# Kernel optimization log

Hardware: AMD Instinct MI355X
Metric: run time of the kernel (lower is better)

## Reference

```python
import jax, jax.numpy as jnp
import numpy as np

B, C, L, H, W = 4, 128, 8, 64, 64

def setup_inputs() -> dict:
    key = jax.random.key(0)
    ks = jax.random.split(key, 9)
    s = 0.05
    return {
        'feats': jax.random.normal(ks[0], (B, C, L, H, W), jnp.float32),
        'proj_w': jax.random.normal(ks[1], (C, C, L), jnp.float32) * s,  # Conv3d kernel (band,1,1) collapsing l
        'proj_b': jax.random.normal(ks[2], (C,), jnp.float32) * s,
        'w1': jax.random.normal(ks[3], (C, C), jnp.float32) * s,
        'b1': jax.random.normal(ks[4], (C,), jnp.float32) * s,
        'w2': jax.random.normal(ks[5], (C, C), jnp.float32) * s,
        'b2': jax.random.normal(ks[6], (C,), jnp.float32) * s,
        'w3': jax.random.normal(ks[7], (C, C), jnp.float32) * s,
        'b3': jax.random.normal(ks[8], (C,), jnp.float32) * s,
        'alpha': jnp.zeros((1,), jnp.float32),
    }

def reference(feats, proj_w, proj_b, w1, b1, w2, b2, w3, b3, alpha):
    b, c, l, h, w = feats.shape
    hw = h * w
    # CVT3D_2D_SA: 3D->2D projection, conv3d kernel (l,1,1) then squeeze
    f2d = jnp.einsum('bclhw,ocl->bohw', feats, proj_w) + proj_b[None, :, None, None]
    # 1x1 conv projections -> (b, c, hw)
    x = f2d.reshape(b, c, hw)
    q = jnp.einsum('bcn,oc->bon', x, w1) + b1[None, :, None]
    k = jnp.einsum('bcn,oc->bon', x, w2) + b2[None, :, None]
    v = jnp.einsum('bcn,oc->bon', x, w3) + b3[None, :, None]
    # scores[b,n,m] = sum_c q[b,c,n] * k[b,c,m]; softmax over m (dim=-1)
    scores = jnp.einsum('bcn,bcm->bnm', q, k)
    attn = jax.nn.softmax(scores, axis=-1)
    # feat_e[b,c,n] = sum_m v[b,c,m] * attn[b,n,m]
    feat_e = jnp.einsum('bcm,bnm->bcn', v, attn).reshape(b, c, h, w)
    # original computes out = alpha*feat_e + f2d but returns feat_e
    return feat_e
```

## Files before the change

kernel.cpp:

```cpp
#include <hip/hip_runtime.h>
#include <stdint.h>

typedef _Float16 h8 __attribute__((ext_vector_type(8)));
typedef _Float16 h4 __attribute__((ext_vector_type(4)));
typedef float f32x4 __attribute__((ext_vector_type(4)));
typedef float f32x16 __attribute__((ext_vector_type(16)));
typedef uint32_t u32x4 __attribute__((ext_vector_type(4)));

#if __has_builtin(__builtin_amdgcn_exp2f)
#define EXP2(x) __builtin_amdgcn_exp2f(x)
#else
#define EXP2(x) exp2f(x)
#endif

#if __has_builtin(__builtin_amdgcn_permlane32_swap)
#define HAVE_PLSWAP 1
#else
#define HAVE_PLSWAP 0
#endif

#define WS_PWH  0u
#define WS_WH   262144u
#define WS_BC   600064u
#define WS_F2D  1048576u
#define WS_OP   5242880u
#define WS_QKVT 38797312u
#define WS_VT   47185920u
#define WS_MLM  0u
#define WS_MLL  524288u

__device__ __forceinline__ void gll16(const void* g, void* l) {
  __builtin_amdgcn_global_load_lds((const __attribute__((address_space(1))) unsigned int*)g,
                                   (__attribute__((address_space(3))) unsigned int*)l, 16, 0, 0);
}

__global__ void k_cvt(const float* __restrict__ pw, const float* __restrict__ pb,
                      const float* __restrict__ w1, const float* __restrict__ b1,
                      const float* __restrict__ w2, const float* __restrict__ b2,
                      const float* __restrict__ w3, const float* __restrict__ b3,
                      _Float16* __restrict__ PWh, _Float16* __restrict__ Wh,
                      float* __restrict__ bc)
{
  const float LOG2E = 1.4426950408889634f;
  int idx = blockIdx.x * 256 + threadIdx.x;
  if (idx < 131072) {
    PWh[idx] = (_Float16)pw[idx];
  } else {
    int j = idx - 131072;
    if (j < 49152) {
      int g = j >> 14, rem = j & 16383;
      const float* wg = (g == 0) ? w1 : (g == 1 ? w2 : w3);
      float v = wg[rem];
      if (g == 0) v *= LOG2E;
      Wh[j] = (_Float16)v;
    }
  }
  if (idx < 384) {
    int g = idx >> 7, o = idx & 127;
    const float* wg = (g == 0) ? w1 : (g == 1 ? w2 : w3);
    const float* bg = (g == 0) ? b1 : (g == 1 ? b2 : b3);
    float s = bg[o];
    for (int c = 0; c < 128; ++c) s += wg[o * 128 + c] * pb[c];
    if (g == 0) s *= LOG2E;
    bc[idx] = s;
  }
}

#define FG1_LDS 51200
__global__ __launch_bounds__(256) void k_fg1(const float* __restrict__ feats,
                                             const _Float16* __restrict__ PWh,
                                             _Float16* __restrict__ f2d)
{
  extern __shared__ char smem[];
  const int t = threadIdx.x, lane = t & 63, w = t >> 6;
  const int lo = lane & 15, hi = lane >> 4;
  const int n0 = blockIdx.x * 32, b = blockIdx.y;
  const int wr = w >> 1, wc = w & 1;
  const char* pwc = (const char*)PWh;

  float4 areg[2];
  auto loadA = [&](int s) {
    #pragma unroll
    for (int p = 0; p < 2; ++p) {
      int i = t + p * 256, row = i >> 3, slot = i & 7;
      areg[p] = *(const float4*)(feats + ((size_t)(b * 1024 + s * 64 + row)) * 4096 + n0 + slot * 4);
    }
  };
  auto writeA = [&](int buf) {
    char* base = smem + buf * 9216;
    #pragma unroll
    for (int p = 0; p < 2; ++p) {
      int i = t + p * 256, row = i >> 3, slot = i & 7;
      *(float4*)(base + row * 144 + slot * 16) = areg[p];
    }
  };
  auto gllB = [&](int s, int buf) {
    char* base = smem + 18432 + buf * 16384;
    #pragma unroll
    for (int q = 0; q < 4; ++q) {
      int o = (w * 4 + q) * 8 + (lane >> 3);
      int slot = lane & 7;
      gll16(pwc + (size_t)o * 2048 + s * 128 + ((slot * 16) ^ ((o & 7) << 4)),
            base + (w * 4 + q) * 1024);
    }
  };

  const f32x4 zero4 = {0.f, 0.f, 0.f, 0.f};
  f32x4 acc[4];
  #pragma unroll
  for (int j2 = 0; j2 < 4; ++j2) acc[j2] = zero4;

  loadA(0); writeA(0); gllB(0, 0);
  for (int s = 0; s < 16; ++s) {
    __syncthreads();
    if (s < 15) { loadA(s + 1); gllB(s + 1, (s + 1) & 1); }
    const char* fb = smem + (s & 1) * 9216;
    const char* pb_ = smem + 18432 + (s & 1) * 16384;
    #pragma unroll
    for (int kk = 0; kk < 2; ++kk) {
      const int nl = wr * 16 + lo;
      float f0 = *(const float*)(fb + (kk * 32 + hi * 8 + 0) * 144 + nl * 4);
      float f1 = *(const float*)(fb + (kk * 32 + hi * 8 + 1) * 144 + nl * 4);
      float f2 = *(const float*)(fb + (kk * 32 + hi * 8 + 2) * 144 + nl * 4);
      float f3 = *(const float*)(fb + (kk * 32 + hi * 8 + 3) * 144 + nl * 4);
      float f4 = *(const float*)(fb + (kk * 32 + hi * 8 + 4) * 144 + nl * 4);
      float f5 = *(const float*)(fb + (kk * 32 + hi * 8 + 5) * 144 + nl * 4);
      float f6 = *(const float*)(fb + (kk * 32 + hi * 8 + 6) * 144 + nl * 4);
      float f7 = *(const float*)(fb + (kk * 32 + hi * 8 + 7) * 144 + nl * 4);
      u32x4 ua = { __builtin_bit_cast(uint32_t, __builtin_amdgcn_cvt_pkrtz(f0, f1)),
                   __builtin_bit_cast(uint32_t, __builtin_amdgcn_cvt_pkrtz(f2, f3)),
                   __builtin_bit_cast(uint32_t, __builtin_amdgcn_cvt_pkrtz(f4, f5)),
                   __builtin_bit_cast(uint32_t, __builtin_amdgcn_cvt_pkrtz(f6, f7)) };
      h8 af = __builtin_bit_cast(h8, ua);
      h8 bf[4];
      #pragma unroll
      for (int j2 = 0; j2 < 4; ++j2) {
        int o = wc * 64 + j2 * 16 + lo;
        bf[j2] = *(const h8*)(pb_ + o * 128 + ((kk * 64 + hi * 16) ^ ((o & 7) << 4)));
      }
      #pragma unroll
      for (int j2 = 0; j2 < 4; ++j2)
        acc[j2] = __builtin_amdgcn_mfma_f32_16x16x32_f16(af, bf[j2], acc[j2], 0, 0, 0);
    }
    if (s < 15) writeA((s + 1) & 1);
  }

  #pragma unroll
  for (int j2 = 0; j2 < 4; ++j2) {
    int o = wc * 64 + j2 * 16 + lo;
    #pragma unroll
    for (int r = 0; r < 4; ++r) {
      int n = n0 + wr * 16 + hi * 4 + r;
      f2d[((size_t)(b * 4096 + n)) * 128 + o] = (_Float16)acc[j2][r];
    }
  }
}

__global__ void k_gemm2(const _Float16* __restrict__ f2d, const _Float16* __restrict__ Wh,
                        const float* __restrict__ bc, _Float16* __restrict__ qkvt,
                        _Float16* __restrict__ vt)
{
  extern __shared__ char smem[];
  const int t = threadIdx.x, lane = t & 63, w = t >> 6;
  const int lo = lane & 15, hi = lane >> 4;
  const int bx = blockIdx.x, n0 = blockIdx.y * 128, b = blockIdx.z;
  const int wr = w >> 1, wc = w & 1;
  const int nb = wr * 64, ob = wc * 64;
  const char* f2c = (const char*)f2d;

  #pragma unroll
  for (int q = 0; q < 8; ++q) {
    int c = w * 8 + q;
    int row = c * 4 + (lane >> 4);
    int col = ((lane & 15) * 16) ^ ((row & 7) << 4);
    gll16(f2c + ((size_t)(b * 4096 + n0 + row)) * 256 + col, smem + c * 1024);
    gll16((const char*)Wh + (size_t)(bx * 128 + row) * 256 + col, smem + 32768 + c * 1024);
  }
  __syncthreads();

  const f32x4 zero4 = {0.f, 0.f, 0.f, 0.f};
  f32x4 acc[4][4];
  #pragma unroll
  for (int i2 = 0; i2 < 4; ++i2)
    #pragma unroll
    for (int j2 = 0; j2 < 4; ++j2) acc[i2][j2] = zero4;

  #pragma unroll
  for (int kk = 0; kk < 4; ++kk) {
    const int cb = kk * 64 + hi * 16;
    h8 af[4], bf[4];
    #pragma unroll
    for (int i2 = 0; i2 < 4; ++i2) {
      int row = nb + i2 * 16 + lo;
      af[i2] = *(const h8*)(smem + row * 256 + (cb ^ ((row & 7) << 4)));
    }
    #pragma unroll
    for (int j2 = 0; j2 < 4; ++j2) {
      int row = ob + j2 * 16 + lo;
      bf[j2] = *(const h8*)(smem + 32768 + row * 256 + (cb ^ ((row & 7) << 4)));
    }
    #pragma unroll
    for (int i2 = 0; i2 < 4; ++i2)
      #pragma unroll
      for (int j2 = 0; j2 < 4; ++j2)
        acc[i2][j2] = __builtin_amdgcn_mfma_f32_16x16x32_f16(af[i2], bf[j2], acc[i2][j2], 0, 0, 0);
  }

  if (bx < 2) {
    #pragma unroll
    for (int j2 = 0; j2 < 4; ++j2) {
      int o = bx * 128 + ob + j2 * 16 + lo;
      float bias = bc[o];
      #pragma unroll
      for (int i2 = 0; i2 < 4; ++i2)
        #pragma unroll
        for (int r = 0; r < 4; ++r) {
          int n = n0 + nb + i2 * 16 + hi * 4 + r;
          qkvt[((size_t)(b * 4096 + n)) * 256 + o] = (_Float16)(acc[i2][j2][r] + bias);
        }
    }
  } else {
    __syncthreads();
    #pragma unroll
    for (int j2 = 0; j2 < 4; ++j2) {
      int o = ob + j2 * 16 + lo;
      float bias = bc[256 + o];
      #pragma unroll
      for (int i2 = 0; i2 < 4; ++i2) {
        int nl = nb + i2 * 16 + hi * 4;
        h4 v4;
        #pragma unroll
        for (int r = 0; r < 4; ++r) v4[r] = (_Float16)(acc[i2][j2][r] + bias);
        *(h4*)(smem + o * 272 + nl * 2) = v4;
      }
    }
    __syncthreads();
    #pragma unroll
    for (int p2 = 0; p2 < 8; ++p2) {
      int i = t + p2 * 256, d = i >> 4, ch = i & 15;
      uint4 v = *(const uint4*)(smem + d * 272 + ch * 16);
      *(uint4*)((char*)vt + ((size_t)(b * 128 + d)) * 8192 + (n0 + ch * 8) * 2) = v;
    }
  }
}

#define ATT_LDS 32768
__global__ __launch_bounds__(256, 2) void k_attn_part(const _Float16* __restrict__ qkvt,
                                                      const _Float16* __restrict__ vt,
                                                      _Float16* __restrict__ opart,
                                                      float* __restrict__ mlm,
                                                      float* __restrict__ mll)
{
  extern __shared__ char smem[];
  const int t = threadIdx.x, lane = t & 63, w = t >> 6;
  const int q31 = lane & 31, h2 = lane >> 5;
  const int id = blockIdx.x;
  const int vid = (id & 7) * 128 + (id >> 3);
  const int qt = vid & 31, bp = vid >> 5;
  const int b = bp >> 3, p = bp & 7;
  const int n0 = qt * 128;
  const char* qbase = (const char*)qkvt + (size_t)b * 4096 * 512;
  const char* vbase = (const char*)vt + (size_t)b * 128 * 8192;

  h8 bq[8];
  {
    const char* qr = qbase + (size_t)(n0 + w * 32 + q31) * 512;
    #pragma unroll
    for (int dk = 0; dk < 8; ++dk) bq[dk] = *(const h8*)(qr + dk * 32 + h2 * 16);
  }

  int koff[2], voff[2], dst_[2];
  #pragma unroll
  for (int i = 0; i < 2; ++i) {
    int idx = t + i * 256;
    int krow = idx >> 4, ks = idx & 15;
    koff[i] = krow * 512 + 256 + ((ks ^ (krow & 7)) * 16);
    int vd = idx >> 2, vs = idx & 3;
    voff[i] = vd * 8192 + ((vs ^ ((vd >> 1) & 3)) * 16);
    dst_[i] = idx * 16;
  }

  auto stage = [&](int m0, int buf) {
    char* kb = smem + buf * 16384;
    char* vb = kb + 8192;
    #pragma unroll
    for (int i = 0; i < 2; ++i) {
      gll16(qbase + (size_t)m0 * 512 + koff[i], kb + dst_[i]);
      gll16(vbase + (size_t)m0 * 2 + voff[i], vb + dst_[i]);
    }
  };

  float m_run = -1e30f, l_run = 0.f;
  f32x16 oacc[4];
  #pragma unroll
  for (int dt = 0; dt < 4; ++dt)
    #pragma unroll
    for (int r = 0; r < 16; ++r) oacc[dt][r] = 0.f;

  const int base = p * 512;
  stage(base, 0);
  __syncthreads();

  for (int it = 0; it < 16; ++it) {
    const int buf = it & 1;
    if (it < 15) stage(base + (it + 1) * 32, buf ^ 1);

    const char* kb = smem + buf * 16384;
    const char* vb = kb + 8192;

    f32x16 s;
    #pragma unroll
    for (int r = 0; r < 16; ++r) s[r] = 0.f;
    __builtin_amdgcn_s_setprio(1);
    #pragma unroll
    for (int dk = 0; dk < 8; ++dk) {
      h8 ak = *(const h8*)(kb + q31 * 256 + (((dk * 2 + h2) ^ (q31 & 7)) * 16));
      s = __builtin_amdgcn_mfma_f32_32x32x16_f16(ak, bq[dk], s, 0, 0, 0);
    }
    __builtin_amdgcn_s_setprio(0);

    float mxl = s[0];
    #pragma unroll
    for (int r = 1; r < 16; ++r) mxl = fmaxf(mxl, s[r]);
    if (__any(mxl > m_run + 8.f)) {
      float mq = fmaxf(mxl, __shfl_xor(mxl, 32));
      float mnew = fmaxf(m_run, mq);
      float scn = EXP2(m_run - mnew);
      m_run = mnew;
      l_run *= scn;
      #pragma unroll
      for (int dt = 0; dt < 4; ++dt)
        #pragma unroll
        for (int r = 0; r < 16; ++r) oacc[dt][r] *= scn;
    }
    float pv[16];
    float rs = 0.f;
    #pragma unroll
    for (int r = 0; r < 16; ++r) { pv[r] = EXP2(s[r] - m_run); rs += pv[r]; }
    l_run += rs;
    uint32_t wd[8];
    #pragma unroll
    for (int j = 0; j < 8; ++j)
      wd[j] = __builtin_bit_cast(uint32_t, __builtin_amdgcn_cvt_pkrtz(pv[2 * j], pv[2 * j + 1]));

#if HAVE_PLSWAP
    auto r02 = __builtin_amdgcn_permlane32_swap(wd[0], wd[2], false, false);
    auto r13 = __builtin_amdgcn_permlane32_swap(wd[1], wd[3], false, false);
    auto r46 = __builtin_amdgcn_permlane32_swap(wd[4], wd[6], false, false);
    auto r57 = __builtin_amdgcn_permlane32_swap(wd[5], wd[7], false, false);
    u32x4 b0 = { r02[0], r13[0], r02[1], r13[1] };
    u32x4 b1 = { r46[0], r57[0], r46[1], r57[1] };
#else
    uint32_t xw[8];
    #pragma unroll
    for (int j = 0; j < 8; ++j) xw[j] = __shfl_xor(wd[j], 32);
    u32x4 b0 = { h2 ? xw[2] : wd[0], h2 ? xw[3] : wd[1],
                 h2 ? wd[2] : xw[0], h2 ? wd[3] : xw[1] };
    u32x4 b1 = { h2 ? xw[6] : wd[4], h2 ? xw[7] : wd[5],
                 h2 ? wd[6] : xw[4], h2 ? wd[7] : xw[5] };
#endif
    h8 bp0 = __builtin_bit_cast(h8, b0);
    h8 bp1 = __builtin_bit_cast(h8, b1);

    __builtin_amdgcn_s_setprio(1);
    #pragma unroll
    for (int ks = 0; ks < 2; ++ks) {
      h8 bpf = ks ? bp1 : bp0;
      #pragma unroll
      for (int dt = 0; dt < 4; ++dt) {
        int d = dt * 32 + q31;
        h8 av = *(const h8*)(vb + d * 64 + (((ks * 2 + h2) ^ ((d >> 1) & 3)) * 16));
        oacc[dt] = __builtin_amdgcn_mfma_f32_32x32x16_f16(av, bpf, oacc[dt], 0, 0, 0);
      }
    }
    __builtin_amdgcn_s_setprio(0);

    if (it < 15) __syncthreads();
  }

  l_run += __shfl_xor(l_run, 32);
  float invl = 1.0f / l_run;
  _Float16* oph = opart + ((size_t)(p * 4 + b) * 128) * 4096;
  const int ncol = n0 + w * 32 + q31;
  #pragma unroll
  for (int dt = 0; dt < 4; ++dt)
    #pragma unroll
    for (int r = 0; r < 16; ++r) {
      int d = dt * 32 + (r & 3) + 8 * (r >> 2) + 4 * h2;
      oph[(size_t)d * 4096 + ncol] = (_Float16)(oacc[dt][r] * invl);
    }
  if (h2 == 0) {
    size_t mlbase = (size_t)(p * 4 + b) * 4096 + ncol;
    mlm[mlbase] = m_run;
    mll[mlbase] = l_run;
  }
}

__global__ void k_reduce(const _Float16* __restrict__ opart, const float* __restrict__ mlm,
                         const float* __restrict__ mll, float* __restrict__ out)
{
  int idx = blockIdx.x * 256 + threadIdx.x;
  int n4 = idx & 1023, d = (idx >> 10) & 127, b = idx >> 17;
  int n0 = n4 * 4;
  f32x4 m[8], lv[8];
  #pragma unroll
  for (int p = 0; p < 8; ++p) {
    size_t mb = (size_t)(p * 4 + b) * 4096 + n0;
    m[p]  = *(const f32x4*)(mlm + mb);
    lv[p] = *(const f32x4*)(mll + mb);
  }
  f32x4 M = m[0];
  #pragma unroll
  for (int p = 1; p < 8; ++p)
    #pragma unroll
    for (int j = 0; j < 4; ++j) M[j] = fmaxf(M[j], m[p][j]);
  f32x4 denom = {0.f, 0.f, 0.f, 0.f}, num = {0.f, 0.f, 0.f, 0.f};
  #pragma unroll
  for (int p = 0; p < 8; ++p) {
    h4 o = *(const h4*)(opart + ((size_t)((p * 4 + b) * 128 + d)) * 4096 + n0);
    #pragma unroll
    for (int j = 0; j < 4; ++j) {
      float wgt = lv[p][j] * EXP2(m[p][j] - M[j]);
      denom[j] += wgt;
      num[j]   += (float)o[j] * wgt;
    }
  }
  f32x4 r;
  #pragma unroll
  for (int j = 0; j < 4; ++j) r[j] = num[j] / denom[j];
  *(f32x4*)(out + ((size_t)(b * 128 + d)) * 4096 + n0) = r;
}

extern "C" void kernel_launch(void* const* d_in, const int* in_sizes, int n_in,
                              void* d_out, int out_size, void* d_ws, size_t ws_size,
                              hipStream_t stream)
{
  const float* feats = (const float*)d_in[0];
  const float* pw = (const float*)d_in[1];
  const float* pb = (const float*)d_in[2];
  const float* w1 = (const float*)d_in[3];
  const float* b1 = (const float*)d_in[4];
  const float* w2 = (const float*)d_in[5];
  const float* b2 = (const float*)d_in[6];
  const float* w3 = (const float*)d_in[7];
  const float* b3 = (const float*)d_in[8];
  char* ws = (char*)d_ws;
  _Float16* PWh = (_Float16*)(ws + WS_PWH);
  _Float16* Wh = (_Float16*)(ws + WS_WH);
  float* bc = (float*)(ws + WS_BC);
  _Float16* f2d = (_Float16*)(ws + WS_F2D);
  _Float16* qkvt = (_Float16*)(ws + WS_QKVT);
  _Float16* vt = (_Float16*)(ws + WS_VT);
  _Float16* opart = (_Float16*)(ws + WS_OP);
  float* mlm = (float*)(ws + WS_MLM);
  float* mll = (float*)(ws + WS_MLL);
  float* out = (float*)d_out;

  hipLaunchKernelGGL(k_cvt, dim3(704), dim3(256), 0, stream,
                     pw, pb, w1, b1, w2, b2, w3, b3, PWh, Wh, bc);
  hipLaunchKernelGGL(k_fg1, dim3(128, 4), dim3(256), FG1_LDS, stream, feats, PWh, f2d);
  hipLaunchKernelGGL(k_gemm2, dim3(3, 32, 4), dim3(256), 65536, stream, f2d, Wh, bc, qkvt, vt);
  hipLaunchKernelGGL(k_attn_part, dim3(1024), dim3(256), ATT_LDS, stream, qkvt, vt, opart, mlm, mll);
  hipLaunchKernelGGL(k_reduce, dim3(2048), dim3(256), 0, stream, opart, mlm, mll, out);
}
```

Before: 104.5 us.

## Process two 32-query tiles per wave in attention to reuse K/V fragments

Each wave now handles 64 queries as two independent 32-row tiles, sharing every K and V LDS fragment load between two MFMA chains. The grid is halved to 512 blocks, with 256 queries per block. This cuts LDS reads and global K/V staging per query and gives the scheduler two independent MFMA streams to interleave. In exchange, accumulator register use roughly doubles, which risks spills or lower occupancy, and fewer blocks means coarser parallelism across the CUs.

```diff
diff --git a/kernel.cpp b/kernel.cpp
--- a/kernel.cpp
+++ b/kernel.cpp
@@ -255,18 +255,22 @@
   const int t = threadIdx.x, lane = t & 63, w = t >> 6;
   const int q31 = lane & 31, h2 = lane >> 5;
   const int id = blockIdx.x;
-  const int vid = (id & 7) * 128 + (id >> 3);
-  const int qt = vid & 31, bp = vid >> 5;
+  const int vid = (id & 7) * 64 + (id >> 3);
+  const int qt = vid & 15, bp = vid >> 4;
   const int b = bp >> 3, p = bp & 7;
-  const int n0 = qt * 128;
+  const int n0 = qt * 256;
   const char* qbase = (const char*)qkvt + (size_t)b * 4096 * 512;
   const char* vbase = (const char*)vt + (size_t)b * 128 * 8192;
 
-  h8 bq[8];
+  h8 bq0[8], bq1[8];
   {
-    const char* qr = qbase + (size_t)(n0 + w * 32 + q31) * 512;
-    #pragma unroll
-    for (int dk = 0; dk < 8; ++dk) bq[dk] = *(const h8*)(qr + dk * 32 + h2 * 16);
+    const char* qr0 = qbase + (size_t)(n0 + w * 64 + q31) * 512;
+    const char* qr1 = qbase + (size_t)(n0 + w * 64 + 32 + q31) * 512;
+    #pragma unroll
+    for (int dk = 0; dk < 8; ++dk) {
+      bq0[dk] = *(const h8*)(qr0 + dk * 32 + h2 * 16);
+      bq1[dk] = *(const h8*)(qr1 + dk * 32 + h2 * 16);
+    }
   }
 
   int koff[2], voff[2], dst_[2];
@@ -290,12 +294,12 @@
     }
   };
 
-  float m_run = -1e30f, l_run = 0.f;
-  f32x16 oacc[4];
+  float m0r = -1e30f, l0r = 0.f, m1r = -1e30f, l1r = 0.f;
+  f32x16 oacc0[4], oacc1[4];
   #pragma unroll
   for (int dt = 0; dt < 4; ++dt)
     #pragma unroll
-    for (int r = 0; r < 16; ++r) oacc[dt][r] = 0.f;
+    for (int r = 0; r < 16; ++r) { oacc0[dt][r] = 0.f; oacc1[dt][r] = 0.f; }
 
   const int base = p * 512;
   stage(base, 0);
@@ -308,69 +312,113 @@
     const char* kb = smem + buf * 16384;
     const char* vb = kb + 8192;
 
-    f32x16 s;
-    #pragma unroll
-    for (int r = 0; r < 16; ++r) s[r] = 0.f;
+    f32x16 s0, s1;
+    #pragma unroll
+    for (int r = 0; r < 16; ++r) { s0[r] = 0.f; s1[r] = 0.f; }
     __builtin_amdgcn_s_setprio(1);
     #pragma unroll
     for (int dk = 0; dk < 8; ++dk) {
       h8 ak = *(const h8*)(kb + q31 * 256 + (((dk * 2 + h2) ^ (q31 & 7)) * 16));
-      s = __builtin_amdgcn_mfma_f32_32x32x16_f16(ak, bq[dk], s, 0, 0, 0);
+      s0 = __builtin_amdgcn_mfma_f32_32x32x16_f16(ak, bq0[dk], s0, 0, 0, 0);
+      s1 = __builtin_amdgcn_mfma_f32_32x32x16_f16(ak, bq1[dk], s1, 0, 0, 0);
     }
     __builtin_amdgcn_s_setprio(0);
 
-    float mxl = s[0];
-    #pragma unroll
-    for (int r = 1; r < 16; ++r) mxl = fmaxf(mxl, s[r]);
-    if (__any(mxl > m_run + 8.f)) {
-      float mq = fmaxf(mxl, __shfl_xor(mxl, 32));
-      float mnew = fmaxf(m_run, mq);
-      float scn = EXP2(m_run - mnew);
-      m_run = mnew;
-      l_run *= scn;
-      #pragma unroll
-      for (int dt = 0; dt < 4; ++dt)
+    h8 p0k0, p0k1, p1k0, p1k1;
+    {
+      float mxl = s0[0];
+      #pragma unroll
+      for (int r = 1; r < 16; ++r) mxl = fmaxf(mxl, s0[r]);
+      if (__any(mxl > m0r + 8.f)) {
+        float mq = fmaxf(mxl, __shfl_xor(mxl, 32));
+        float mnew = fmaxf(m0r, mq);
+        float scn = EXP2(m0r - mnew);
+        m0r = mnew;
+        l0r *= scn;
         #pragma unroll
-        for (int r = 0; r < 16; ++r) oacc[dt][r] *= scn;
-    }
-    float pv[16];
-    float rs = 0.f;
-    #pragma unroll
-    for (int r = 0; r < 16; ++r) { pv[r] = EXP2(s[r] - m_run); rs += pv[r]; }
-    l_run += rs;
-    uint32_t wd[8];
-    #pragma unroll
-    for (int j = 0; j < 8; ++j)
-      wd[j] = __builtin_bit_cast(uint32_t, __builtin_amdgcn_cvt_pkrtz(pv[2 * j], pv[2 * j + 1]));
-
+        for (int dt = 0; dt < 4; ++dt)
+          #pragma unroll
+          for (int r = 0; r < 16; ++r) oacc0[dt][r] *= scn;
+      }
+      float pv[16], rs = 0.f;
+      #pragma unroll
+      for (int r = 0; r < 16; ++r) { pv[r] = EXP2(s0[r] - m0r); rs += pv[r]; }
+      l0r += rs;
+      uint32_t wd[8];
+      #pragma unroll
+      for (int j = 0; j < 8; ++j)
+        wd[j] = __builtin_bit_cast(uint32_t, __builtin_amdgcn_cvt_pkrtz(pv[2 * j], pv[2 * j + 1]));
 #if HAVE_PLSWAP
-    auto r02 = __builtin_amdgcn_permlane32_swap(wd[0], wd[2], false, false);
-    auto r13 = __builtin_amdgcn_permlane32_swap(wd[1], wd[3], false, false);
-    auto r46 = __builtin_amdgcn_permlane32_swap(wd[4], wd[6], false, false);
-    auto r57 = __builtin_amdgcn_permlane32_swap(wd[5], wd[7], false, false);
-    u32x4 b0 = { r02[0], r13[0], r02[1], r13[1] };
-    u32x4 b1 = { r46[0], r57[0], r46[1], r57[1] };
+      auto r02 = __builtin_amdgcn_permlane32_swap(wd[0], wd[2], false, false);
+      auto r13 = __builtin_amdgcn_permlane32_swap(wd[1], wd[3], false, false);
+      auto r46 = __builtin_amdgcn_permlane32_swap(wd[4], wd[6], false, false);
+      auto r57 = __builtin_amdgcn_permlane32_swap(wd[5], wd[7], false, false);
+      u32x4 b0 = { r02[0], r13[0], r02[1], r13[1] };
+      u32x4 b1 = { r46[0], r57[0], r46[1], r57[1] };
 #else
-    uint32_t xw[8];
-    #pragma unroll
-    for (int j = 0; j < 8; ++j) xw[j] = __shfl_xor(wd[j], 32);
-    u32x4 b0 = { h2 ? xw[2] : wd[0], h2 ? xw[3] : wd[1],
-                 h2 ? wd[2] : xw[0], h2 ? wd[3] : xw[1] };
-    u32x4 b1 = { h2 ? xw[6] : wd[4], h2 ? xw[7] : wd[5],
-                 h2 ? wd[6] : xw[4], h2 ? wd[7] : xw[5] };
+      uint32_t xw[8];
+      #pragma unroll
+      for (int j = 0; j < 8; ++j) xw[j] = __shfl_xor(wd[j], 32);
+      u32x4 b0 = { h2 ? xw[2] : wd[0], h2 ? xw[3] : wd[1],
+                   h2 ? wd[2] : xw[0], h2 ? wd[3] : xw[1] };
+      u32x4 b1 = { h2 ? xw[6] : wd[4], h2 ? xw[7] : wd[5],
+                   h2 ? wd[6] : xw[4], h2 ? wd[7] : xw[5] };
 #endif
-    h8 bp0 = __builtin_bit_cast(h8, b0);
-    h8 bp1 = __builtin_bit_cast(h8, b1);
+      p0k0 = __builtin_bit_cast(h8, b0);
+      p0k1 = __builtin_bit_cast(h8, b1);
+    }
+    {
+      float mxl = s1[0];
+      #pragma unroll
+      for (int r = 1; r < 16; ++r) mxl = fmaxf(mxl, s1[r]);
+      if (__any(mxl > m1r + 8.f)) {
+        float mq = fmaxf(mxl, __shfl_xor(mxl, 32));
+        float mnew = fmaxf(m1r, mq);
+        float scn = EXP2(m1r - mnew);
+        m1r = mnew;
+        l1r *= scn;
+        #pragma unroll
+        for (int dt = 0; dt < 4; ++dt)
+          #pragma unroll
+          for (int r = 0; r < 16; ++r) oacc1[dt][r] *= scn;
+      }
+      float pv[16], rs = 0.f;
+      #pragma unroll
+      for (int r = 0; r < 16; ++r) { pv[r] = EXP2(s1[r] - m1r); rs += pv[r]; }
+      l1r += rs;
+      uint32_t wd[8];
+      #pragma unroll
+      for (int j = 0; j < 8; ++j)
+        wd[j] = __builtin_bit_cast(uint32_t, __builtin_amdgcn_cvt_pkrtz(pv[2 * j], pv[2 * j + 1]));
+#if HAVE_PLSWAP
+      auto r02 = __builtin_amdgcn_permlane32_swap(wd[0], wd[2], false, false);
+      auto r13 = __builtin_amdgcn_permlane32_swap(wd[1], wd[3], false, false);
+      auto r46 = __builtin_amdgcn_permlane32_swap(wd[4], wd[6], false, false);
+      auto r57 = __builtin_amdgcn_permlane32_swap(wd[5], wd[7], false, false);
+      u32x4 b0 = { r02[0], r13[0], r02[1], r13[1] };
+      u32x4 b1 = { r46[0], r57[0], r46[1], r57[1] };
+#else
+      uint32_t xw[8];
+      #pragma unroll
+      for (int j = 0; j < 8; ++j) xw[j] = __shfl_xor(wd[j], 32);
+      u32x4 b0 = { h2 ? xw[2] : wd[0], h2 ? xw[3] : wd[1],
+                   h2 ? wd[2] : xw[0], h2 ? wd[3] : xw[1] };
+      u32x4 b1 = { h2 ? xw[6] : wd[4], h2 ? xw[7] : wd[5],
+                   h2 ? wd[6] : xw[4], h2 ? wd[7] : xw[5] };
+#endif
+      p1k0 = __builtin_bit_cast(h8, b0);
+      p1k1 = __builtin_bit_cast(h8, b1);
+    }
 
     __builtin_amdgcn_s_setprio(1);
     #pragma unroll
     for (int ks = 0; ks < 2; ++ks) {
-      h8 bpf = ks ? bp1 : bp0;
       #pragma unroll
       for (int dt = 0; dt < 4; ++dt) {
         int d = dt * 32 + q31;
         h8 av = *(const h8*)(vb + d * 64 + (((ks * 2 + h2) ^ ((d >> 1) & 3)) * 16));
-        oacc[dt] = __builtin_amdgcn_mfma_f32_32x32x16_f16(av, bpf, oacc[dt], 0, 0, 0);
+        oacc0[dt] = __builtin_amdgcn_mfma_f32_32x32x16_f16(av, ks ? p0k1 : p0k0, oacc0[dt], 0, 0, 0);
+        oacc1[dt] = __builtin_amdgcn_mfma_f32_32x32x16_f16(av, ks ? p1k1 : p1k0, oacc1[dt], 0, 0, 0);
       }
     }
     __builtin_amdgcn_s_setprio(0);
@@ -378,21 +426,23 @@
     if (it < 15) __syncthreads();
   }
 
-  l_run += __shfl_xor(l_run, 32);
-  float invl = 1.0f / l_run;
   _Float16* oph = opart + ((size_t)(p * 4 + b) * 128) * 4096;
-  const int ncol = n0 + w * 32 + q31;
+  l0r += __shfl_xor(l0r, 32);
+  l1r += __shfl_xor(l1r, 32);
+  float inv0 = 1.0f / l0r, inv1 = 1.0f / l1r;
+  const int nc0 = n0 + w * 64 + q31, nc1 = nc0 + 32;
   #pragma unroll
   for (int dt = 0; dt < 4; ++dt)
     #pragma unroll
     for (int r = 0; r < 16; ++r) {
       int d = dt * 32 + (r & 3) + 8 * (r >> 2) + 4 * h2;
-      oph[(size_t)d * 4096 + ncol] = (_Float16)(oacc[dt][r] * invl);
+      oph[(size_t)d * 4096 + nc0] = (_Float16)(oacc0[dt][r] * inv0);
+      oph[(size_t)d * 4096 + nc1] = (_Float16)(oacc1[dt][r] * inv1);
     }
   if (h2 == 0) {
-    size_t mlbase = (size_t)(p * 4 + b) * 4096 + ncol;
-    mlm[mlbase] = m_run;
-    mll[mlbase] = l_run;
+    size_t mlb = (size_t)(p * 4 + b) * 4096;
+    mlm[mlb + nc0] = m0r;  mll[mlb + nc0] = l0r;
+    mlm[mlb + nc1] = m1r;  mll[mlb + nc1] = l1r;
   }
 }
 
@@ -460,6 +510,6 @@
                      pw, pb, w1, b1, w2, b2, w3, b3, PWh, Wh, bc);
   hipLaunchKernelGGL(k_fg1, dim3(128, 4), dim3(256), FG1_LDS, stream, feats, PWh, f2d);
   hipLaunchKernelGGL(k_gemm2, dim3(3, 32, 4), dim3(256), 65536, stream, f2d, Wh, bc, qkvt, vt);
-  hipLaunchKernelGGL(k_attn_part, dim3(1024), dim3(256), ATT_LDS, stream, qkvt, vt, opart, mlm, mll);
+  hipLaunchKernelGGL(k_attn_part, dim3(512), dim3(256), ATT_LDS, stream, qkvt, vt, opart, mlm, mll);
   hipLaunchKernelGGL(k_reduce, dim3(2048), dim3(256), 0, stream, opart, mlm, mll, out);
 }
```

Result: slower. 107.0 us (+2.4%).
